# Kernel optimization log

Hardware: AMD Instinct MI355X
Metric: run time of the kernel (lower is better)

Reference implementation:

```python
import jax, jax.numpy as jnp
import numpy as np

B, S, D, H = 2, 2048, 1024, 16
DEPTH = D // H


def setup_inputs() -> dict:
    key = jax.random.key(0)
    ks = jax.random.split(key, 8)
    w_scale = 0.02
    # causal mask: 1.0 where attention is NOT allowed (added as mask * -1e9)
    causal = jnp.triu(jnp.ones((S, S), dtype=jnp.float32), k=1)[None, None]  # [1,1,S,S]
    return {
        "q": jax.random.normal(ks[0], (B, S, D), dtype=jnp.float32),
        "k": jax.random.normal(ks[1], (B, S, D), dtype=jnp.float32),
        "v": jax.random.normal(ks[2], (B, S, D), dtype=jnp.float32),
        "mask": causal,
        "Wq": jax.random.normal(ks[3], (D, D), dtype=jnp.float32) * w_scale,
        "bq": jnp.zeros((D,), dtype=jnp.float32),
        "Wk": jax.random.normal(ks[4], (D, D), dtype=jnp.float32) * w_scale,
        "bk": jnp.zeros((D,), dtype=jnp.float32),
        "Wv": jax.random.normal(ks[5], (D, D), dtype=jnp.float32) * w_scale,
        "bv": jnp.zeros((D,), dtype=jnp.float32),
        "Wo": jax.random.normal(ks[6], (D, D), dtype=jnp.float32) * w_scale,
        "bo": jnp.zeros((D,), dtype=jnp.float32),
    }


def _split_heads(x):
    # [B,S,D] -> [B,H,S,depth]
    return x.reshape(B, S, H, DEPTH).transpose(0, 2, 1, 3)


def reference(q, k, v, mask, Wq, bq, Wk, bk, Wv, bv, Wo, bo):
    qh = _split_heads(q @ Wq + bq)
    kh = _split_heads(k @ Wk + bk)
    vh = _split_heads(v @ Wv + bv)
    scale = 1.0 / jnp.sqrt(jnp.asarray(DEPTH, dtype=qh.dtype))
    logits = jnp.einsum('bhqd,bhkd->bhqk', qh, kh) * scale  # [B,H,S,S]
    logits = logits + mask * (-1e9)
    attn = jax.nn.softmax(logits, axis=-1)
    out = jnp.einsum('bhqk,bhkd->bhqd', attn, vh)  # [B,H,S,depth]
    out = out.transpose(0, 2, 1, 3).reshape(B, S, D)
    return out @ Wo + bo
```

## Files before the change

kernel.cpp:

```cpp
#include <hip/hip_runtime.h>


typedef unsigned short u16;
typedef unsigned int u32;

using bf16x8 = __attribute__((ext_vector_type(8))) short;
using f32x4  = __attribute__((ext_vector_type(4))) float;

#define SEQ 2048
#define DMODEL 1024
#define NHEAD 16
#define DEPTH 64
#define BATCH 2
#define M_ROWS (BATCH * SEQ)

__device__ __forceinline__ u16 f2bf(float f) {
    union { float f; u32 u; } v; v.f = f;
    u32 u = v.u;
    return (u16)((u + 0x7FFFu + ((u >> 16) & 1u)) >> 16);
}
__device__ __forceinline__ u16 f2bf_trunc(float f) {
    union { float f; u32 u; } v; v.f = f;
    return (u16)(v.u >> 16);
}

__device__ __forceinline__ f32x4 mfma16(bf16x8 a, bf16x8 b, f32x4 c) {
    return __builtin_amdgcn_mfma_f32_16x16x32_bf16(a, b, c, 0, 0, 0);
}

__device__ __forceinline__ void glds16(const u16* src, u16* dst) {
    __builtin_amdgcn_global_load_lds((const __attribute__((address_space(1))) void*)src,
                                     (__attribute__((address_space(3))) void*)dst,
                                     16, 0, 0);
}

__device__ __forceinline__ bf16x8 fragld(const u16* base, int lr, int gc) {
    return *(const bf16x8*)(base + lr * 64 + (((gc ^ lr) & 7) << 3));
}

__global__ void cvt3_kernel(const float* __restrict__ q, const float* __restrict__ k,
                            const float* __restrict__ v,
                            u16* __restrict__ qo, u16* __restrict__ ko, u16* __restrict__ vo) {
    const float* in; u16* out;
    if (blockIdx.z == 0)      { in = q; out = qo; }
    else if (blockIdx.z == 1) { in = k; out = ko; }
    else                      { in = v; out = vo; }
    int idx = blockIdx.x * blockDim.x + threadIdx.x;
    float4 val = ((const float4*)in)[idx];
    ushort4 o;
    o.x = f2bf(val.x); o.y = f2bf(val.y); o.z = f2bf(val.z); o.w = f2bf(val.w);
    ((ushort4*)out)[idx] = o;
}

__global__ void wtrans_kernel(const float* __restrict__ Wq, const float* __restrict__ Wk,
                              const float* __restrict__ Wv, const float* __restrict__ Wo,
                              u16* __restrict__ Wqt, u16* __restrict__ Wkt,
                              u16* __restrict__ Wvt, u16* __restrict__ Wot) {
    __shared__ float tile[32][33];
    const float* W; u16* Wt;
    switch (blockIdx.z) {
        case 0: W = Wq; Wt = Wqt; break;
        case 1: W = Wk; Wt = Wkt; break;
        case 2: W = Wv; Wt = Wvt; break;
        default: W = Wo; Wt = Wot; break;
    }
    int k0 = blockIdx.x * 32, n0 = blockIdx.y * 32;
    int tx = threadIdx.x, ty = threadIdx.y;
#pragma unroll
    for (int i = 0; i < 4; ++i)
        tile[ty + 8 * i][tx] = W[(size_t)(k0 + ty + 8 * i) * DMODEL + n0 + tx];
    __syncthreads();
#pragma unroll
    for (int i = 0; i < 4; ++i)
        Wt[(size_t)(n0 + ty + 8 * i) * DMODEL + k0 + tx] = f2bf(tile[tx][ty + 8 * i]);
}

template<int TM>
__device__ __forceinline__ void gemm_core(const u16* __restrict__ A, const u16* __restrict__ Bt,
                                          const float* __restrict__ bias,
                                          u16* __restrict__ outb, float* __restrict__ outf,
                                          int mode, float oscale, int bm0, int bn0) {
    constexpr int K = DMODEL;
    constexpr int MI = TM / 32;
    __shared__ u16 As[TM * 64];
    __shared__ u16 Bs[128 * 64];
    int t = threadIdx.x;
    int w = t >> 6, lane = t & 63, l15 = lane & 15, quad = lane >> 4;
    int wm = (w >> 1) * (TM / 2), wn = (w & 1) * 64;
    int r8 = lane >> 3, g8 = lane & 7;
    int gswz = ((g8 ^ r8) << 3);
    f32x4 acc[MI][4] = {};

    for (int it = 0; it < K / 64; ++it) {
        int k0 = it * 64;
        __syncthreads();
#pragma unroll
        for (int c = 0; c < MI; ++c) {
            int ch = w * MI + c;
            glds16(A + (size_t)(bm0 + ch * 8 + r8) * K + k0 + gswz, As + ch * 512);
        }
#pragma unroll
        for (int c = 0; c < 4; ++c) {
            int ch = w * 4 + c;
            glds16(Bt + (size_t)(bn0 + ch * 8 + r8) * K + k0 + gswz, Bs + ch * 512);
        }
        __syncthreads();
#pragma unroll
        for (int kk = 0; kk < 2; ++kk) {
            bf16x8 af[MI], bfr[4];
#pragma unroll
            for (int i = 0; i < MI; ++i) af[i]  = fragld(As, wm + i * 16 + l15, kk * 4 + quad);
#pragma unroll
            for (int j = 0; j < 4;  ++j) bfr[j] = fragld(Bs, wn + j * 16 + l15, kk * 4 + quad);
#pragma unroll
            for (int i = 0; i < MI; ++i)
#pragma unroll
                for (int j = 0; j < 4; ++j)
                    acc[i][j] = mfma16(af[i], bfr[j], acc[i][j]);
        }
    }
#pragma unroll
    for (int i = 0; i < MI; ++i) {
        int row_g0 = bm0 + wm + i * 16 + quad * 4;
#pragma unroll
        for (int j = 0; j < 4; ++j) {
            int col_g = bn0 + wn + j * 16 + l15;
            float bsv = bias[col_g];
#pragma unroll
            for (int r = 0; r < 4; ++r) {
                float v = (acc[i][j][r] + bsv) * oscale;
                int rg = row_g0 + r;
                if (mode == 2) {
                    outf[(size_t)rg * DMODEL + col_g] = v;
                } else {
                    int b = rg >> 11, s = rg & (SEQ - 1);
                    int h = col_g >> 6, d = col_g & 63;
                    size_t idx;
                    if (mode == 0) idx = ((size_t)(b * NHEAD + h) * SEQ + s) * DEPTH + d;
                    else           idx = ((size_t)(b * NHEAD + h) * DEPTH + d) * SEQ + s;
                    outb[idx] = f2bf(v);
                }
            }
        }
    }
}

#define SCALE_Q 0.1803368801111204f

__global__ __launch_bounds__(256) void gemm_qkv(
        const u16* __restrict__ qb, const u16* __restrict__ kb, const u16* __restrict__ vb,
        const u16* __restrict__ Wqt, const u16* __restrict__ Wkt, const u16* __restrict__ Wvt,
        const float* __restrict__ bq, const float* __restrict__ bk, const float* __restrict__ bv,
        u16* __restrict__ Qp, u16* __restrict__ Kp, u16* __restrict__ Vpt) {
    int id = blockIdx.x;
    int c = id & 7, m = id >> 3;
    int slab = c * 12 + (m >> 3);
    int x = m & 7;
    int z = slab >> 5, y = slab & 31;
    int bm0 = y * 128, bn0 = x * 128;
    if (z == 0)      gemm_core<128>(qb, Wqt, bq, Qp,  nullptr, 0, SCALE_Q, bm0, bn0);
    else if (z == 1) gemm_core<128>(kb, Wkt, bk, Kp,  nullptr, 0, 1.0f,    bm0, bn0);
    else             gemm_core<128>(vb, Wvt, bv, Vpt, nullptr, 1, 1.0f,    bm0, bn0);
}

__global__ __launch_bounds__(256) void gemm_out(
        const u16* __restrict__ attnb, const u16* __restrict__ Wot,
        const float* __restrict__ bo, float* __restrict__ out) {
    int id = blockIdx.x;
    int c = id & 7, m = id >> 3;
    int slab = c * 8 + (m >> 3);
    int x = m & 7;
    gemm_core<64>(attnb, Wot, bo, nullptr, out, 2, 1.0f, slab * 64, x * 128);
}

#define LP 72
__global__ __launch_bounds__(256) void attn_kernel(
        const u16* __restrict__ Qp, const u16* __restrict__ Kp,
        const u16* __restrict__ Vpt, u16* __restrict__ attn_out) {
    __shared__ u16 Klds[2][64 * 64];
    __shared__ u16 Vtlds[2][64 * 64];
    __shared__ u16 Plds[4 * 16 * LP];
    int t = threadIdx.x, w = t >> 6, lane = t & 63, l15 = lane & 15, quad = lane >> 4;
    int r8 = lane >> 3, g8 = lane & 7;
    int gswz = ((g8 ^ r8) << 3);
    u16* Pw = Plds + w * 16 * LP;

    int id = blockIdx.x;
    int c = id & 7, m = id >> 3;
    int bh = c * 4 + (m >> 4);
    int pair = m & 15;
    int b = bh >> 4, h = bh & 15;
    const u16* Qbase = Qp  + (size_t)bh * SEQ * DEPTH;
    const u16* Kbase = Kp  + (size_t)bh * SEQ * DEPTH;
    const u16* Vbase = Vpt + (size_t)bh * DEPTH * SEQ;

#pragma unroll
    for (int phase = 0; phase < 2; ++phase) {
        int qt = phase ? (31 - pair) : pair;
        int q0 = qt * 64;
        int nkt = qt + 1;

        int qrow = q0 + w * 16 + l15;
        bf16x8 qf[2];
        qf[0] = *(const bf16x8*)(Qbase + (size_t)qrow * DEPTH + quad * 8);
        qf[1] = *(const bf16x8*)(Qbase + (size_t)qrow * DEPTH + 32 + quad * 8);

        f32x4 of[4] = {};
        float l4[4] = {0.f, 0.f, 0.f, 0.f};

        __syncthreads();
#pragma unroll
        for (int c2 = 0; c2 < 2; ++c2) {
            int ch = w * 2 + c2;
            glds16(Kbase + (size_t)(ch * 8 + r8) * DEPTH + gswz, Klds[0] + ch * 512);
            glds16(Vbase + (size_t)(ch * 8 + r8) * SEQ + gswz,   Vtlds[0] + ch * 512);
        }

        for (int kt = 0; kt < nkt; ++kt) {
            int cur = kt & 1;
            __syncthreads();
            if (kt + 1 < nkt) {
                int nx = cur ^ 1, kn = kt + 1;
#pragma unroll
                for (int c2 = 0; c2 < 2; ++c2) {
                    int ch = w * 2 + c2;
                    glds16(Kbase + (size_t)(kn * 64 + ch * 8 + r8) * DEPTH + gswz,
                           Klds[nx] + ch * 512);
                    glds16(Vbase + (size_t)(ch * 8 + r8) * SEQ + kn * 64 + gswz,
                           Vtlds[nx] + ch * 512);
                }
            }
            f32x4 sc[4] = {};
#pragma unroll
            for (int nt = 0; nt < 4; ++nt)
#pragma unroll
                for (int kk = 0; kk < 2; ++kk)
                    sc[nt] = mfma16(qf[kk], fragld(Klds[cur], nt * 16 + l15, kk * 4 + quad), sc[nt]);

            bool diag = (kt == nkt - 1);
#pragma unroll
            for (int nt = 0; nt < 4; ++nt) {
#pragma unroll
                for (int r = 0; r < 4; ++r) {
                    float e = exp2f(sc[nt][r]);
                    if (diag) {
                        int col = nt * 16 + l15, row_ = w * 16 + quad * 4 + r;
                        e = (col > row_) ? 0.f : e;
                    }
                    l4[r] += e;
                    Pw[(quad * 4 + r) * LP + nt * 16 + l15] = f2bf_trunc(e);
                }
            }
            bf16x8 pf[2];
            pf[0] = *(const bf16x8*)(Pw + l15 * LP + quad * 8);
            pf[1] = *(const bf16x8*)(Pw + l15 * LP + 32 + quad * 8);
#pragma unroll
            for (int nt = 0; nt < 4; ++nt)
#pragma unroll
                for (int kk = 0; kk < 2; ++kk)
                    of[nt] = mfma16(pf[kk], fragld(Vtlds[cur], nt * 16 + l15, kk * 4 + quad), of[nt]);
        }
#pragma unroll
        for (int r = 0; r < 4; ++r) {
#pragma unroll
            for (int off = 1; off < 16; off <<= 1)
                l4[r] += __shfl_xor(l4[r], off, 64);
        }
#pragma unroll
        for (int r = 0; r < 4; ++r) {
            float inv = 1.0f / l4[r];
            int s_ = q0 + w * 16 + quad * 4 + r;
#pragma unroll
            for (int nt = 0; nt < 4; ++nt) {
                int dcol = h * DEPTH + nt * 16 + l15;
                attn_out[((size_t)(b * SEQ + s_)) * DMODEL + dcol] = f2bf(of[nt][r] * inv);
            }
        }
    }
}

extern "C" void kernel_launch(void* const* d_in, const int* in_sizes, int n_in,
                              void* d_out, int out_size, void* d_ws, size_t ws_size,
                              hipStream_t stream) {
    const float* q  = (const float*)d_in[0];
    const float* k  = (const float*)d_in[1];
    const float* v  = (const float*)d_in[2];
    const float* Wq = (const float*)d_in[4];
    const float* bq = (const float*)d_in[5];
    const float* Wk = (const float*)d_in[6];
    const float* bk = (const float*)d_in[7];
    const float* Wv = (const float*)d_in[8];
    const float* bv = (const float*)d_in[9];
    const float* Wo = (const float*)d_in[10];
    const float* bo = (const float*)d_in[11];
    float* out = (float*)d_out;

    char* ws = (char*)d_ws;
    const size_t SZ_ACT = (size_t)M_ROWS * DMODEL * 2;
    const size_t SZ_W   = (size_t)DMODEL * DMODEL * 2;
    u16* qb   = (u16*)(ws);
    u16* kb   = (u16*)(ws + SZ_ACT);
    u16* vb   = (u16*)(ws + 2 * SZ_ACT);
    u16* Wqt  = (u16*)(ws + 3 * SZ_ACT);
    u16* Wkt  = (u16*)(ws + 3 * SZ_ACT + SZ_W);
    u16* Wvt  = (u16*)(ws + 3 * SZ_ACT + 2 * SZ_W);
    u16* Wot  = (u16*)(ws + 3 * SZ_ACT + 3 * SZ_W);
    u16* Qp   = (u16*)(ws + 3 * SZ_ACT + 4 * SZ_W);
    u16* Kp   = (u16*)(ws + 4 * SZ_ACT + 4 * SZ_W);
    u16* Vpt  = (u16*)(ws + 5 * SZ_ACT + 4 * SZ_W);
    u16* attnb= (u16*)(ws + 6 * SZ_ACT + 4 * SZ_W);

    cvt3_kernel<<<dim3(4096, 1, 3), 256, 0, stream>>>(q, k, v, qb, kb, vb);
    wtrans_kernel<<<dim3(32, 32, 4), dim3(32, 8), 0, stream>>>(Wq, Wk, Wv, Wo, Wqt, Wkt, Wvt, Wot);
    gemm_qkv<<<dim3(768), 256, 0, stream>>>(
        qb, kb, vb, Wqt, Wkt, Wvt, bq, bk, bv, Qp, Kp, Vpt);
    attn_kernel<<<dim3(512), 256, 0, stream>>>(Qp, Kp, Vpt, attnb);
    gemm_out<<<dim3(512), 256, 0, stream>>>(attnb, Wot, bo, out);
}
```

Baseline: 239.7 us.

## Use atomic per-XCD work queue for causal attention tiles and MFMA row sums

Replaces the fixed pair-balanced mapping of query tiles to blocks with a persistent scheme. Each block pulls work items from a per-XCD atomic counter, taking the largest causal tiles first and keeping each XCD on its own four heads for L2 locality. The softmax row sum is now accumulated with an extra MFMA against a ones vector, replacing per-element adds and cross-lane shuffles. The cost is atomic traffic, a memset before the launch, and more launched blocks, which exit once the queue is empty.

```diff
diff --git a/kernel.cpp b/kernel.cpp
--- a/kernel.cpp
+++ b/kernel.cpp
@@ -176,29 +176,35 @@
 #define LP 72
 __global__ __launch_bounds__(256) void attn_kernel(
         const u16* __restrict__ Qp, const u16* __restrict__ Kp,
-        const u16* __restrict__ Vpt, u16* __restrict__ attn_out) {
+        const u16* __restrict__ Vpt, u16* __restrict__ attn_out, u32* __restrict__ ctrs) {
     __shared__ u16 Klds[2][64 * 64];
     __shared__ u16 Vtlds[2][64 * 64];
     __shared__ u16 Plds[4 * 16 * LP];
+    __shared__ u32 item_s;
     int t = threadIdx.x, w = t >> 6, lane = t & 63, l15 = lane & 15, quad = lane >> 4;
     int r8 = lane >> 3, g8 = lane & 7;
     int gswz = ((g8 ^ r8) << 3);
     u16* Pw = Plds + w * 16 * LP;
-
-    int id = blockIdx.x;
-    int c = id & 7, m = id >> 3;
-    int bh = c * 4 + (m >> 4);
-    int pair = m & 15;
-    int b = bh >> 4, h = bh & 15;
-    const u16* Qbase = Qp  + (size_t)bh * SEQ * DEPTH;
-    const u16* Kbase = Kp  + (size_t)bh * SEQ * DEPTH;
-    const u16* Vbase = Vpt + (size_t)bh * DEPTH * SEQ;
-
-#pragma unroll
-    for (int phase = 0; phase < 2; ++phase) {
-        int qt = phase ? (31 - pair) : pair;
+    int xcd = blockIdx.x & 7;
+    u32* my_ctr = ctrs + xcd * 32;
+
+    bf16x8 ones;
+#pragma unroll
+    for (int i = 0; i < 8; ++i) ones[i] = (short)0x3F80;
+
+    for (;;) {
+        if (t == 0) item_s = atomicAdd(my_ctr, 1);
+        __syncthreads();
+        u32 item = item_s;
+        if (item >= 128) break;
+        int qt = 31 - (int)(item >> 2);
+        int bh = xcd * 4 + (int)(item & 3);
         int q0 = qt * 64;
         int nkt = qt + 1;
+        int b = bh >> 4, h = bh & 15;
+        const u16* Qbase = Qp  + (size_t)bh * SEQ * DEPTH;
+        const u16* Kbase = Kp  + (size_t)bh * SEQ * DEPTH;
+        const u16* Vbase = Vpt + (size_t)bh * DEPTH * SEQ;
 
         int qrow = q0 + w * 16 + l15;
         bf16x8 qf[2];
@@ -206,9 +212,8 @@
         qf[1] = *(const bf16x8*)(Qbase + (size_t)qrow * DEPTH + 32 + quad * 8);
 
         f32x4 of[4] = {};
-        float l4[4] = {0.f, 0.f, 0.f, 0.f};
-
-        __syncthreads();
+        f32x4 lacc = {};
+
 #pragma unroll
         for (int c2 = 0; c2 < 2; ++c2) {
             int ch = w * 2 + c2;
@@ -247,7 +252,6 @@
                         int col = nt * 16 + l15, row_ = w * 16 + quad * 4 + r;
                         e = (col > row_) ? 0.f : e;
                     }
-                    l4[r] += e;
                     Pw[(quad * 4 + r) * LP + nt * 16 + l15] = f2bf_trunc(e);
                 }
             }
@@ -255,20 +259,16 @@
             pf[0] = *(const bf16x8*)(Pw + l15 * LP + quad * 8);
             pf[1] = *(const bf16x8*)(Pw + l15 * LP + 32 + quad * 8);
 #pragma unroll
-            for (int nt = 0; nt < 4; ++nt)
-#pragma unroll
-                for (int kk = 0; kk < 2; ++kk)
+            for (int kk = 0; kk < 2; ++kk) {
+                lacc = mfma16(pf[kk], ones, lacc);
+#pragma unroll
+                for (int nt = 0; nt < 4; ++nt)
                     of[nt] = mfma16(pf[kk], fragld(Vtlds[cur], nt * 16 + l15, kk * 4 + quad), of[nt]);
+            }
         }
 #pragma unroll
         for (int r = 0; r < 4; ++r) {
-#pragma unroll
-            for (int off = 1; off < 16; off <<= 1)
-                l4[r] += __shfl_xor(l4[r], off, 64);
-        }
-#pragma unroll
-        for (int r = 0; r < 4; ++r) {
-            float inv = 1.0f / l4[r];
+            float inv = 1.0f / lacc[r];
             int s_ = q0 + w * 16 + quad * 4 + r;
 #pragma unroll
             for (int nt = 0; nt < 4; ++nt) {
@@ -309,11 +309,13 @@
     u16* Kp   = (u16*)(ws + 4 * SZ_ACT + 4 * SZ_W);
     u16* Vpt  = (u16*)(ws + 5 * SZ_ACT + 4 * SZ_W);
     u16* attnb= (u16*)(ws + 6 * SZ_ACT + 4 * SZ_W);
-
+    u32* ctrs = (u32*)(ws + 7 * SZ_ACT + 4 * SZ_W);
+
+    hipMemsetAsync(ctrs, 0, 1024, stream);
     cvt3_kernel<<<dim3(4096, 1, 3), 256, 0, stream>>>(q, k, v, qb, kb, vb);
     wtrans_kernel<<<dim3(32, 32, 4), dim3(32, 8), 0, stream>>>(Wq, Wk, Wv, Wo, Wqt, Wkt, Wvt, Wot);
     gemm_qkv<<<dim3(768), 256, 0, stream>>>(
         qb, kb, vb, Wqt, Wkt, Wvt, bq, bk, bv, Qp, Kp, Vpt);
-    attn_kernel<<<dim3(512), 256, 0, stream>>>(Qp, Kp, Vpt, attnb);
+    attn_kernel<<<dim3(768), 256, 0, stream>>>(Qp, Kp, Vpt, attnb, ctrs);
     gemm_out<<<dim3(512), 256, 0, stream>>>(attnb, Wot, bo, out);
 }
```

Result: no change. 237.2 us (-1.1%).

## Use two-wave attention blocks with 32 query rows per wave and MFMA row sums

Applied to the files above, without the earlier changes.

The attention kernel now runs 128 threads per block, with each wave handling two 16-row query groups. Each K and V fragment read from LDS is reused across both groups, halving fragment loads per MFMA. The softmax denominator is now computed by an MFMA of P against a vector of ones instead of scalar adds and shuffles, which also makes it use the same bf16-rounded P as the PV product. The cost is more registers per wave and fewer waves per block for latency hiding.

```diff
diff --git a/kernel.cpp b/kernel.cpp
--- a/kernel.cpp
+++ b/kernel.cpp
@@ -173,45 +173,52 @@
     gemm_core<64>(attnb, Wot, bo, nullptr, out, 2, 1.0f, slab * 64, x * 128);
 }
 
-#define LP 72
-__global__ __launch_bounds__(256) void attn_kernel(
+#define LPW 68
+__global__ __launch_bounds__(128) void attn_kernel(
         const u16* __restrict__ Qp, const u16* __restrict__ Kp,
         const u16* __restrict__ Vpt, u16* __restrict__ attn_out) {
     __shared__ u16 Klds[2][64 * 64];
     __shared__ u16 Vtlds[2][64 * 64];
-    __shared__ u16 Plds[4 * 16 * LP];
+    __shared__ u16 Plds[2 * 32 * LPW];
     int t = threadIdx.x, w = t >> 6, lane = t & 63, l15 = lane & 15, quad = lane >> 4;
     int r8 = lane >> 3, g8 = lane & 7;
     int gswz = ((g8 ^ r8) << 3);
-    u16* Pw = Plds + w * 16 * LP;
+    u16* Pw = Plds + w * 32 * LPW;
 
     int id = blockIdx.x;
-    int c = id & 7, m = id >> 3;
-    int bh = c * 4 + (m >> 4);
+    int xcd = id & 7, m = id >> 3;
+    int bh = xcd * 4 + (m >> 4);
     int pair = m & 15;
     int b = bh >> 4, h = bh & 15;
     const u16* Qbase = Qp  + (size_t)bh * SEQ * DEPTH;
     const u16* Kbase = Kp  + (size_t)bh * SEQ * DEPTH;
     const u16* Vbase = Vpt + (size_t)bh * DEPTH * SEQ;
 
+    bf16x8 ones;
+#pragma unroll
+    for (int i = 0; i < 8; ++i) ones[i] = (short)0x3F80;
+
 #pragma unroll
     for (int phase = 0; phase < 2; ++phase) {
         int qt = phase ? (31 - pair) : pair;
         int q0 = qt * 64;
         int nkt = qt + 1;
 
-        int qrow = q0 + w * 16 + l15;
-        bf16x8 qf[2];
-        qf[0] = *(const bf16x8*)(Qbase + (size_t)qrow * DEPTH + quad * 8);
-        qf[1] = *(const bf16x8*)(Qbase + (size_t)qrow * DEPTH + 32 + quad * 8);
-
-        f32x4 of[4] = {};
-        float l4[4] = {0.f, 0.f, 0.f, 0.f};
+        bf16x8 qf[2][2];
+#pragma unroll
+        for (int g = 0; g < 2; ++g) {
+            const u16* qp = Qbase + (size_t)(q0 + w * 32 + g * 16 + l15) * DEPTH + quad * 8;
+            qf[g][0] = *(const bf16x8*)(qp);
+            qf[g][1] = *(const bf16x8*)(qp + 32);
+        }
+
+        f32x4 of[2][4] = {};
+        f32x4 lacc[2] = {};
 
         __syncthreads();
 #pragma unroll
-        for (int c2 = 0; c2 < 2; ++c2) {
-            int ch = w * 2 + c2;
+        for (int c2 = 0; c2 < 4; ++c2) {
+            int ch = w * 4 + c2;
             glds16(Kbase + (size_t)(ch * 8 + r8) * DEPTH + gswz, Klds[0] + ch * 512);
             glds16(Vbase + (size_t)(ch * 8 + r8) * SEQ + gswz,   Vtlds[0] + ch * 512);
         }
@@ -222,60 +229,74 @@
             if (kt + 1 < nkt) {
                 int nx = cur ^ 1, kn = kt + 1;
 #pragma unroll
-                for (int c2 = 0; c2 < 2; ++c2) {
-                    int ch = w * 2 + c2;
+                for (int c2 = 0; c2 < 4; ++c2) {
+                    int ch = w * 4 + c2;
                     glds16(Kbase + (size_t)(kn * 64 + ch * 8 + r8) * DEPTH + gswz,
                            Klds[nx] + ch * 512);
                     glds16(Vbase + (size_t)(ch * 8 + r8) * SEQ + kn * 64 + gswz,
                            Vtlds[nx] + ch * 512);
                 }
             }
-            f32x4 sc[4] = {};
+            f32x4 sc[2][4] = {};
 #pragma unroll
             for (int nt = 0; nt < 4; ++nt)
 #pragma unroll
+                for (int kk = 0; kk < 2; ++kk) {
+                    bf16x8 kf = fragld(Klds[cur], nt * 16 + l15, kk * 4 + quad);
+#pragma unroll
+                    for (int g = 0; g < 2; ++g)
+                        sc[g][nt] = mfma16(qf[g][kk], kf, sc[g][nt]);
+                }
+
+            bool diag = (kt == nkt - 1);
+#pragma unroll
+            for (int g = 0; g < 2; ++g)
+#pragma unroll
+                for (int nt = 0; nt < 4; ++nt)
+#pragma unroll
+                    for (int r = 0; r < 4; ++r) {
+                        float e = exp2f(sc[g][nt][r]);
+                        if (diag) {
+                            int col = nt * 16 + l15;
+                            int row_ = w * 32 + g * 16 + quad * 4 + r;
+                            e = (col > row_) ? 0.f : e;
+                        }
+                        Pw[(g * 16 + quad * 4 + r) * LPW + nt * 16 + l15] = f2bf_trunc(e);
+                    }
+            bf16x8 pf[2][2];
+#pragma unroll
+            for (int g = 0; g < 2; ++g) {
+                pf[g][0] = *(const bf16x8*)(Pw + (g * 16 + l15) * LPW + quad * 8);
+                pf[g][1] = *(const bf16x8*)(Pw + (g * 16 + l15) * LPW + 32 + quad * 8);
+            }
+#pragma unroll
+            for (int g = 0; g < 2; ++g)
+#pragma unroll
                 for (int kk = 0; kk < 2; ++kk)
-                    sc[nt] = mfma16(qf[kk], fragld(Klds[cur], nt * 16 + l15, kk * 4 + quad), sc[nt]);
-
-            bool diag = (kt == nkt - 1);
-#pragma unroll
-            for (int nt = 0; nt < 4; ++nt) {
-#pragma unroll
-                for (int r = 0; r < 4; ++r) {
-                    float e = exp2f(sc[nt][r]);
-                    if (diag) {
-                        int col = nt * 16 + l15, row_ = w * 16 + quad * 4 + r;
-                        e = (col > row_) ? 0.f : e;
-                    }
-                    l4[r] += e;
-                    Pw[(quad * 4 + r) * LP + nt * 16 + l15] = f2bf_trunc(e);
+                    lacc[g] = mfma16(pf[g][kk], ones, lacc[g]);
+#pragma unroll
+            for (int nt = 0; nt < 4; ++nt)
+#pragma unroll
+                for (int kk = 0; kk < 2; ++kk) {
+                    bf16x8 vf = fragld(Vtlds[cur], nt * 16 + l15, kk * 4 + quad);
+#pragma unroll
+                    for (int g = 0; g < 2; ++g)
+                        of[g][nt] = mfma16(pf[g][kk], vf, of[g][nt]);
+                }
+        }
+#pragma unroll
+        for (int g = 0; g < 2; ++g)
+#pragma unroll
+            for (int r = 0; r < 4; ++r) {
+                float inv = 1.0f / lacc[g][r];
+                int s_ = q0 + w * 32 + g * 16 + quad * 4 + r;
+#pragma unroll
+                for (int nt = 0; nt < 4; ++nt) {
+                    int dcol = h * DEPTH + nt * 16 + l15;
+                    attn_out[((size_t)(b * SEQ + s_)) * DMODEL + dcol] =
+                        f2bf(of[g][nt][r] * inv);
                 }
             }
-            bf16x8 pf[2];
-            pf[0] = *(const bf16x8*)(Pw + l15 * LP + quad * 8);
-            pf[1] = *(const bf16x8*)(Pw + l15 * LP + 32 + quad * 8);
-#pragma unroll
-            for (int nt = 0; nt < 4; ++nt)
-#pragma unroll
-                for (int kk = 0; kk < 2; ++kk)
-                    of[nt] = mfma16(pf[kk], fragld(Vtlds[cur], nt * 16 + l15, kk * 4 + quad), of[nt]);
-        }
-#pragma unroll
-        for (int r = 0; r < 4; ++r) {
-#pragma unroll
-            for (int off = 1; off < 16; off <<= 1)
-                l4[r] += __shfl_xor(l4[r], off, 64);
-        }
-#pragma unroll
-        for (int r = 0; r < 4; ++r) {
-            float inv = 1.0f / l4[r];
-            int s_ = q0 + w * 16 + quad * 4 + r;
-#pragma unroll
-            for (int nt = 0; nt < 4; ++nt) {
-                int dcol = h * DEPTH + nt * 16 + l15;
-                attn_out[((size_t)(b * SEQ + s_)) * DMODEL + dcol] = f2bf(of[nt][r] * inv);
-            }
-        }
     }
 }
 
@@ -314,6 +335,6 @@
     wtrans_kernel<<<dim3(32, 32, 4), dim3(32, 8), 0, stream>>>(Wq, Wk, Wv, Wo, Wqt, Wkt, Wvt, Wot);
     gemm_qkv<<<dim3(768), 256, 0, stream>>>(
         qb, kb, vb, Wqt, Wkt, Wvt, bq, bk, bv, Qp, Kp, Vpt);
-    attn_kernel<<<dim3(512), 256, 0, stream>>>(Qp, Kp, Vpt, attnb);
+    attn_kernel<<<dim3(512), 128, 0, stream>>>(Qp, Kp, Vpt, attnb);
     gemm_out<<<dim3(512), 256, 0, stream>>>(attnb, Wot, bo, out);
 }
```

New measurement: 260.3 us. 8.6% more time.
